# Kernel tuning notes

Hardware: AMD Instinct MI355X
Metric: run time of the kernel (lower is better)

## Reference

```python
import jax, jax.numpy as jnp
import numpy as np

B, N, H, BD, P = 16, 128, 128, 64, 256

def setup_inputs() -> dict:
    key = jax.random.key(0)
    ks = jax.random.split(key, 10)
    s = lambda fan_in: 1.0 / np.sqrt(fan_in)
    return {
        "hidden_states": jax.random.normal(ks[0], (B, N, H), dtype=jnp.float32),
        "positions": jax.random.normal(ks[1], (B, N, 2), dtype=jnp.float32),
        "W1": jax.random.uniform(ks[2], (2, BD), jnp.float32, -s(2), s(2)),
        "b1": jax.random.uniform(ks[3], (BD,), jnp.float32, -s(2), s(2)),
        "W2": jax.random.uniform(ks[4], (H + BD, P), jnp.float32, -s(H + BD), s(H + BD)),
        "b2": jax.random.uniform(ks[5], (P,), jnp.float32, -s(H + BD), s(H + BD)),
        "W3": jax.random.uniform(ks[6], (P, P), jnp.float32, -s(P), s(P)),
        "b3": jax.random.uniform(ks[7], (P,), jnp.float32, -s(P), s(P)),
        "Wout": jax.random.uniform(ks[8], (P, P), jnp.float32, -s(P), s(P)),
        "bout": jax.random.uniform(ks[9], (P,), jnp.float32, -s(P), s(P)),
    }

def reference(hidden_states, positions, W1, b1, W2, b2, W3, b3, Wout, bout):
    b, n, h = hidden_states.shape
    # rel[b,i,j] = pos[b,j] - pos[b,i]  -> [B,N,N,2]
    rel = positions[:, None, :, :] - positions[:, :, None, :]
    enc = jax.nn.relu(rel @ W1 + b1)                       # [B,N,N,BD]
    hid = jnp.broadcast_to(hidden_states[:, None, :, :], (b, n, n, h))
    x = jnp.concatenate([hid, enc], axis=-1)               # [B,N,N,H+BD]
    emb = jax.nn.relu(x @ W2 + b2) @ W3 + b3               # [B,N,N,P]
    # mask self (j == i) with -inf before max-pool over neighbors j
    self_mask = jnp.eye(n, dtype=bool)[None, :, :, None]
    emb = jnp.where(self_mask, -jnp.inf, emb)
    pooled = emb.max(axis=2)                               # [B,N,P]
    return pooled @ Wout + bout
```

## Files before the change

### kernel.cpp

```cpp
#include <hip/hip_runtime.h>
#include <hip/hip_fp16.h>

using f16x4 = __attribute__((ext_vector_type(4))) _Float16;
using f16x8 = __attribute__((ext_vector_type(8))) _Float16;
using f32x4 = __attribute__((ext_vector_type(4))) float;

__device__ __forceinline__ f16x4 ld_f16x4(const void* p) {
    return *reinterpret_cast<const f16x4*>(p);
}
__device__ __forceinline__ f16x8 ld_f16x8(const void* p) {
    return *reinterpret_cast<const f16x8*>(p);
}

__global__ void sp_wconv(const float* __restrict__ W2, const float* __restrict__ W3,
                         const float* __restrict__ pos, const float* __restrict__ W1,
                         const float* __restrict__ b1,
                         _Float16* __restrict__ W2bt, _Float16* __restrict__ W3s,
                         _Float16* __restrict__ T1h, _Float16* __restrict__ T1bh) {
    int t = blockIdx.x * 256 + threadIdx.x;
    if (t < 16384) {
        int p = t >> 6, k = t & 63;
        W2bt[t] = (_Float16)W2[(128 + k) * 256 + p];
    }
    {
        int ks = t >> 13, rem = t & 8191;
        int row = rem >> 5, inner = rem & 31;
        int slot = inner >> 3, e = inner & 7;
        int g = slot ^ ((row >> 1) & 3);
        int k = ks * 32 + ((e & 4) << 2) + (g << 2) + (e & 3);
        W3s[t] = (_Float16)W3[k * 256 + row];
    }
#pragma unroll
    for (int h = 0; h < 2; ++h) {
        int idx = t + h * 65536;
        int row = idx >> 6, k = idx & 63;
        float v = pos[row * 2] * W1[k] + pos[row * 2 + 1] * W1[64 + k];
        T1h[idx]  = (_Float16)v;
        T1bh[idx] = (_Float16)(v + b1[k]);
    }
}

__global__ void sp_hpart(const float* __restrict__ hs, const float* __restrict__ W2,
                         const float* __restrict__ b2, _Float16* __restrict__ hp16) {
    __shared__ float sh[8 * 128];
    int rb = blockIdx.x * 8;
    int tid = threadIdx.x;
    for (int t = tid; t < 1024; t += 256) sh[t] = hs[rb * 128 + t];
    __syncthreads();
    float acc[8];
    float bb = b2[tid];
#pragma unroll
    for (int r = 0; r < 8; ++r) acc[r] = bb;
    for (int k = 0; k < 128; ++k) {
        float w = W2[k * 256 + tid];
#pragma unroll
        for (int r = 0; r < 8; ++r) acc[r] += sh[r * 128 + k] * w;
    }
#pragma unroll
    for (int r = 0; r < 8; ++r) hp16[(rb + r) * 256 + tid] = (_Float16)acc[r];
}

__global__ __launch_bounds__(256, 2) void sp_main(
    const float* __restrict__ b3,
    const _Float16* __restrict__ hp16, const _Float16* __restrict__ W2bt,
    const _Float16* __restrict__ W3s, const _Float16* __restrict__ T1h,
    const _Float16* __restrict__ T1bh, float* __restrict__ pool) {
    __shared__ __align__(16) char sW3[8][8192];
    __shared__ _Float16 sPoolH[4][8][128];

    const int bid = blockIdx.x;
    const int ig = bid & 15, ph = (bid >> 4) & 1, b = bid >> 5;
    const int tid = threadIdx.x;
    const int wj = tid >> 6, lane = tid & 63;
    const int l15 = lane & 15, lk = lane >> 4;

    {
        const uint4* W3v = (const uint4*)W3s + ph * 512;
        uint4* dst = (uint4*)sW3;
#pragma unroll
        for (int c = 0; c < 16; ++c) {
            dst[c * 256 + tid] = W3v[c * 256 + tid + (c >> 1) * 512];
        }
    }

    f16x8 tb[2][2];
#pragma unroll
    for (int jt = 0; jt < 2; ++jt) {
        int j = wj * 32 + jt * 16 + l15;
        const _Float16* tj = T1bh + (b * 128 + j) * 64 + lk * 8;
        tb[jt][0] = ld_f16x8(tj);
        tb[jt][1] = ld_f16x8(tj + 32);
    }

    const _Float16* hpb = hp16 + (b * 128 + wj * 32 + l15) * 256 + lk * 4;
    const _Float16* tib = T1h + (b * 128) * 64 + lk * 8;
    const int slot = lk ^ ((l15 >> 1) & 3);

    __syncthreads();

#pragma unroll 1
    for (int ii2 = 0; ii2 < 4; ++ii2) {
        const int i0 = ig * 8 + ii2 * 2;
        const int i1 = i0 + 1;

        const _Float16* w2p = W2bt;
        const _Float16* hpp = hpb;
        asm volatile("" : "+v"(w2p), "+v"(hpp));

        f16x8 benc[2][2][2];
#pragma unroll
        for (int iq = 0; iq < 2; ++iq) {
            const int i = iq ? i1 : i0;
#pragma unroll
            for (int s32 = 0; s32 < 2; ++s32) {
                f16x8 cv = ld_f16x8(tib + i * 64 + s32 * 32);
#pragma unroll
                for (int jt = 0; jt < 2; ++jt) {
                    f16x8 v;
#pragma unroll
                    for (int e = 0; e < 8; ++e) {
                        _Float16 d = tb[jt][s32][e] - cv[e];
                        v[e] = d > (_Float16)0 ? d : (_Float16)0;
                    }
                    benc[iq][jt][s32] = v;
                }
            }
        }

        f32x4 eacc[2][2][8];
#pragma unroll
        for (int iq = 0; iq < 2; ++iq)
#pragma unroll
            for (int jt = 0; jt < 2; ++jt)
#pragma unroll
                for (int pt = 0; pt < 8; ++pt)
                    eacc[iq][jt][pt] = (f32x4){0.f, 0.f, 0.f, 0.f};

#pragma unroll
        for (int ks = 0; ks < 8; ++ks) {
            f16x8 u[2][2];
#pragma unroll
            for (int pp = 0; pp < 2; ++pp) {
                const int pt = ks * 2 + pp;
                f32x4 a[2][2];
#pragma unroll
                for (int iq = 0; iq < 2; ++iq)
#pragma unroll
                    for (int jt = 0; jt < 2; ++jt) a[iq][jt] = (f32x4){0.f, 0.f, 0.f, 0.f};
#pragma unroll
                for (int s32 = 0; s32 < 2; ++s32) {
                    f16x8 aw = ld_f16x8(w2p + (pt * 16 + l15) * 64 + s32 * 32 + lk * 8);
                    a[0][0] = __builtin_amdgcn_mfma_f32_16x16x32_f16(aw, benc[0][0][s32], a[0][0], 0, 0, 0);
                    a[0][1] = __builtin_amdgcn_mfma_f32_16x16x32_f16(aw, benc[0][1][s32], a[0][1], 0, 0, 0);
                    a[1][0] = __builtin_amdgcn_mfma_f32_16x16x32_f16(aw, benc[1][0][s32], a[1][0], 0, 0, 0);
                    a[1][1] = __builtin_amdgcn_mfma_f32_16x16x32_f16(aw, benc[1][1][s32], a[1][1], 0, 0, 0);
                }
                f16x4 h0 = ld_f16x4(hpp + pt * 16);
                f16x4 h1 = ld_f16x4(hpp + 16 * 256 + pt * 16);
#pragma unroll
                for (int iq = 0; iq < 2; ++iq)
#pragma unroll
                    for (int r = 0; r < 4; ++r) {
                        float t0 = a[iq][0][r] + (float)h0[r];
                        float t1 = a[iq][1][r] + (float)h1[r];
                        u[iq][0][pp * 4 + r] = (_Float16)(t0 > 0.f ? t0 : 0.f);
                        u[iq][1][pp * 4 + r] = (_Float16)(t1 > 0.f ? t1 : 0.f);
                    }
            }
#pragma unroll
            for (int pt = 0; pt < 8; ++pt) {
                f16x8 bf = ld_f16x8(sW3[ks] + (pt * 16 + l15) * 64 + slot * 16);
                eacc[0][0][pt] = __builtin_amdgcn_mfma_f32_16x16x32_f16(u[0][0], bf, eacc[0][0][pt], 0, 0, 0);
                eacc[0][1][pt] = __builtin_amdgcn_mfma_f32_16x16x32_f16(u[0][1], bf, eacc[0][1][pt], 0, 0, 0);
                eacc[1][0][pt] = __builtin_amdgcn_mfma_f32_16x16x32_f16(u[1][0], bf, eacc[1][0][pt], 0, 0, 0);
                eacc[1][1][pt] = __builtin_amdgcn_mfma_f32_16x16x32_f16(u[1][1], bf, eacc[1][1][pt], 0, 0, 0);
            }
        }

#pragma unroll
        for (int iq = 0; iq < 2; ++iq) {
            const int i = iq ? i1 : i0;
#pragma unroll
            for (int pt = 0; pt < 8; ++pt) {
                float m = -INFINITY;
#pragma unroll
                for (int jt = 0; jt < 2; ++jt) {
#pragma unroll
                    for (int r = 0; r < 4; ++r) {
                        int row = wj * 32 + jt * 16 + lk * 4 + r;
                        float v = eacc[iq][jt][pt][r];
                        if (row != i) m = fmaxf(m, v);
                    }
                }
                m = fmaxf(m, __shfl_xor(m, 16));
                m = fmaxf(m, __shfl_xor(m, 32));
                if (lane < 16) sPoolH[wj][ii2 * 2 + iq][pt * 16 + l15] = (_Float16)m;
            }
        }
    }
    __syncthreads();

#pragma unroll
    for (int q = 0; q < 4; ++q) {
        int idx = q * 256 + tid;
        int ii = idx >> 7, t = idx & 127;
        float v = fmaxf(fmaxf((float)sPoolH[0][ii][t], (float)sPoolH[1][ii][t]),
                        fmaxf((float)sPoolH[2][ii][t], (float)sPoolH[3][ii][t]));
        int p = ph * 128 + t;
        pool[(b * 128 + ig * 8 + ii) * 256 + p] = v + b3[p];
    }
}

__global__ void sp_out(const float* __restrict__ Wout, const float* __restrict__ bout,
                       float* __restrict__ io) {
    __shared__ float sp[8 * 256];
    int rb = blockIdx.x * 8;
    int tid = threadIdx.x;
    for (int t = tid; t < 2048; t += 256) sp[t] = io[rb * 256 + t];
    __syncthreads();
    float acc[8];
    float bb = bout[tid];
#pragma unroll
    for (int r = 0; r < 8; ++r) acc[r] = bb;
    for (int k = 0; k < 256; ++k) {
        float w = Wout[k * 256 + tid];
#pragma unroll
        for (int r = 0; r < 8; ++r) acc[r] += sp[r * 256 + k] * w;
    }
#pragma unroll
    for (int r = 0; r < 8; ++r) io[(rb + r) * 256 + tid] = acc[r];
}

extern "C" void kernel_launch(void* const* d_in, const int* in_sizes, int n_in,
                              void* d_out, int out_size, void* d_ws, size_t ws_size,
                              hipStream_t stream) {
    const float* hs   = (const float*)d_in[0];
    const float* pos  = (const float*)d_in[1];
    const float* W1   = (const float*)d_in[2];
    const float* b1   = (const float*)d_in[3];
    const float* W2   = (const float*)d_in[4];
    const float* b2   = (const float*)d_in[5];
    const float* W3   = (const float*)d_in[6];
    const float* b3   = (const float*)d_in[7];
    const float* Wout = (const float*)d_in[8];
    const float* bout = (const float*)d_in[9];
    float* out = (float*)d_out;

    _Float16* hp16 = (_Float16*)d_ws;
    _Float16* W2bt = (_Float16*)((char*)d_ws + (1 << 20));
    _Float16* W3s  = (_Float16*)((char*)d_ws + (1 << 20) + 32768);
    _Float16* T1h  = (_Float16*)((char*)d_ws + (1 << 20) + 32768 + 131072);
    _Float16* T1bh = (_Float16*)((char*)d_ws + (1 << 20) + 32768 + 131072 + 262144);

    sp_wconv<<<256, 256, 0, stream>>>(W2, W3, pos, W1, b1, W2bt, W3s, T1h, T1bh);
    sp_hpart<<<256, 256, 0, stream>>>(hs, W2, b2, hp16);
    sp_main<<<512, 256, 0, stream>>>(b3, hp16, W2bt, W3s, T1h, T1bh, out);
    sp_out<<<256, 256, 0, stream>>>(Wout, bout, out);
}
```

Before: 99.73 us.

## Switch main kernel MFMAs from 16x16x32 to 32x32x16 tiles

Rewrites the fused two-layer MLP inner loop to use 32x32x16 f16 MFMA instructions instead of 16x16x32, with a matching re-swizzle of the W3 shared-memory layout and of the lane-to-row mappings for the encoding, hidden-part and pooling steps. The larger tiles are meant to reduce operand loads and instruction count per FLOP and to cut the cross-lane shuffles in the max-pool. The bias-add and ReLU on the first-layer output are now done in half precision rather than float, which loses some accuracy. The larger accumulator tiles also raise register pressure under the 2-blocks-per-CU launch bound.

```diff
diff --git a/kernel.cpp b/kernel.cpp
--- a/kernel.cpp
+++ b/kernel.cpp
@@ -4,6 +4,7 @@
 using f16x4 = __attribute__((ext_vector_type(4))) _Float16;
 using f16x8 = __attribute__((ext_vector_type(8))) _Float16;
 using f32x4 = __attribute__((ext_vector_type(4))) float;
+using f32x16 = __attribute__((ext_vector_type(16))) float;
 
 __device__ __forceinline__ f16x4 ld_f16x4(const void* p) {
     return *reinterpret_cast<const f16x4*>(p);
@@ -23,11 +24,11 @@
         W2bt[t] = (_Float16)W2[(128 + k) * 256 + p];
     }
     {
-        int ks = t >> 13, rem = t & 8191;
-        int row = rem >> 5, inner = rem & 31;
+        int kk = t >> 12, rem = t & 4095;
+        int row = rem >> 4, inner = rem & 15;
         int slot = inner >> 3, e = inner & 7;
-        int g = slot ^ ((row >> 1) & 3);
-        int k = ks * 32 + ((e & 4) << 2) + (g << 2) + (e & 3);
+        int h = slot ^ ((row >> 2) & 1);
+        int k = kk * 16 + (e & 3) + 8 * (e >> 2) + 4 * h;
         W3s[t] = (_Float16)W3[k * 256 + row];
     }
 #pragma unroll
@@ -65,36 +66,28 @@
     const _Float16* __restrict__ hp16, const _Float16* __restrict__ W2bt,
     const _Float16* __restrict__ W3s, const _Float16* __restrict__ T1h,
     const _Float16* __restrict__ T1bh, float* __restrict__ pool) {
-    __shared__ __align__(16) char sW3[8][8192];
+    __shared__ __align__(16) char sW3[16][4096];
     __shared__ _Float16 sPoolH[4][8][128];
 
     const int bid = blockIdx.x;
     const int ig = bid & 15, ph = (bid >> 4) & 1, b = bid >> 5;
     const int tid = threadIdx.x;
     const int wj = tid >> 6, lane = tid & 63;
-    const int l15 = lane & 15, lk = lane >> 4;
+    const int l31 = lane & 31, hi = lane >> 5;
 
     {
-        const uint4* W3v = (const uint4*)W3s + ph * 512;
+        const uint4* W3v = (const uint4*)W3s;
         uint4* dst = (uint4*)sW3;
 #pragma unroll
-        for (int c = 0; c < 16; ++c) {
-            dst[c * 256 + tid] = W3v[c * 256 + tid + (c >> 1) * 512];
-        }
-    }
-
-    f16x8 tb[2][2];
-#pragma unroll
-    for (int jt = 0; jt < 2; ++jt) {
-        int j = wj * 32 + jt * 16 + l15;
-        const _Float16* tj = T1bh + (b * 128 + j) * 64 + lk * 8;
-        tb[jt][0] = ld_f16x8(tj);
-        tb[jt][1] = ld_f16x8(tj + 32);
-    }
-
-    const _Float16* hpb = hp16 + (b * 128 + wj * 32 + l15) * 256 + lk * 4;
-    const _Float16* tib = T1h + (b * 128) * 64 + lk * 8;
-    const int slot = lk ^ ((l15 >> 1) & 3);
+        for (int c = 0; c < 16; ++c)
+            dst[c * 256 + tid] = W3v[c * 512 + ph * 256 + tid];
+    }
+
+    const int jl = wj * 32 + l31;
+    const _Float16* tjb = T1bh + (b * 128 + jl) * 64 + hi * 8;
+    const _Float16* tib = T1h + (b * 128) * 64 + hi * 8;
+    const _Float16* hpb = hp16 + (b * 128 + jl) * 256;
+    const int slotB = (hi ^ ((l31 >> 2) & 1)) * 16;
 
     __syncthreads();
 
@@ -107,94 +100,83 @@
         const _Float16* hpp = hpb;
         asm volatile("" : "+v"(w2p), "+v"(hpp));
 
-        f16x8 benc[2][2][2];
+        f16x8 benc[2][4];
+#pragma unroll
+        for (int s = 0; s < 4; ++s) {
+            f16x8 tbv = ld_f16x8(tjb + s * 16);
+            f16x8 cv0 = ld_f16x8(tib + i0 * 64 + s * 16);
+            f16x8 cv1 = ld_f16x8(tib + i1 * 64 + s * 16);
+#pragma unroll
+            for (int e = 0; e < 8; ++e) {
+                _Float16 d0 = tbv[e] - cv0[e];
+                _Float16 d1 = tbv[e] - cv1[e];
+                benc[0][s][e] = d0 > (_Float16)0 ? d0 : (_Float16)0;
+                benc[1][s][e] = d1 > (_Float16)0 ? d1 : (_Float16)0;
+            }
+        }
+
+        f32x16 eacc[2][4];
+#pragma unroll
+        for (int iq = 0; iq < 2; ++iq)
+#pragma unroll
+            for (int nt = 0; nt < 4; ++nt)
+#pragma unroll
+                for (int r = 0; r < 16; ++r) eacc[iq][nt][r] = 0.f;
+
+#pragma unroll
+        for (int t = 0; t < 8; ++t) {
+            f32x16 a0, a1;
+#pragma unroll
+            for (int r = 0; r < 16; ++r) { a0[r] = 0.f; a1[r] = 0.f; }
+#pragma unroll
+            for (int s = 0; s < 4; ++s) {
+                f16x8 aw = ld_f16x8(w2p + (t * 32 + l31) * 64 + s * 16 + hi * 8);
+                a0 = __builtin_amdgcn_mfma_f32_32x32x16_f16(aw, benc[0][s], a0, 0, 0, 0);
+                a1 = __builtin_amdgcn_mfma_f32_32x32x16_f16(aw, benc[1][s], a1, 0, 0, 0);
+            }
+            f16x4 hp0 = ld_f16x4(hpp + t * 32 + 4 * hi);
+            f16x4 hp1 = ld_f16x4(hpp + t * 32 + 8 + 4 * hi);
+            f16x4 hp2 = ld_f16x4(hpp + t * 32 + 16 + 4 * hi);
+            f16x4 hp3 = ld_f16x4(hpp + t * 32 + 24 + 4 * hi);
+            f16x8 u00, u01, u10, u11;
+#pragma unroll
+            for (int e = 0; e < 4; ++e) {
+                _Float16 v;
+                v = (_Float16)a0[e]      + hp0[e]; u00[e]     = v > (_Float16)0 ? v : (_Float16)0;
+                v = (_Float16)a0[e + 4]  + hp1[e]; u00[e + 4] = v > (_Float16)0 ? v : (_Float16)0;
+                v = (_Float16)a0[e + 8]  + hp2[e]; u01[e]     = v > (_Float16)0 ? v : (_Float16)0;
+                v = (_Float16)a0[e + 12] + hp3[e]; u01[e + 4] = v > (_Float16)0 ? v : (_Float16)0;
+                v = (_Float16)a1[e]      + hp0[e]; u10[e]     = v > (_Float16)0 ? v : (_Float16)0;
+                v = (_Float16)a1[e + 4]  + hp1[e]; u10[e + 4] = v > (_Float16)0 ? v : (_Float16)0;
+                v = (_Float16)a1[e + 8]  + hp2[e]; u11[e]     = v > (_Float16)0 ? v : (_Float16)0;
+                v = (_Float16)a1[e + 12] + hp3[e]; u11[e + 4] = v > (_Float16)0 ? v : (_Float16)0;
+            }
+#pragma unroll
+            for (int nt = 0; nt < 4; ++nt) {
+                const char* rowp = (const char*)sW3 + (nt * 32 + l31) * 32 + slotB;
+                f16x8 bf0 = ld_f16x8(rowp + (2 * t) * 4096);
+                f16x8 bf1 = ld_f16x8(rowp + (2 * t + 1) * 4096);
+                eacc[0][nt] = __builtin_amdgcn_mfma_f32_32x32x16_f16(u00, bf0, eacc[0][nt], 0, 0, 0);
+                eacc[1][nt] = __builtin_amdgcn_mfma_f32_32x32x16_f16(u10, bf0, eacc[1][nt], 0, 0, 0);
+                eacc[0][nt] = __builtin_amdgcn_mfma_f32_32x32x16_f16(u01, bf1, eacc[0][nt], 0, 0, 0);
+                eacc[1][nt] = __builtin_amdgcn_mfma_f32_32x32x16_f16(u11, bf1, eacc[1][nt], 0, 0, 0);
+            }
+        }
+
 #pragma unroll
         for (int iq = 0; iq < 2; ++iq) {
             const int i = iq ? i1 : i0;
 #pragma unroll
-            for (int s32 = 0; s32 < 2; ++s32) {
-                f16x8 cv = ld_f16x8(tib + i * 64 + s32 * 32);
-#pragma unroll
-                for (int jt = 0; jt < 2; ++jt) {
-                    f16x8 v;
-#pragma unroll
-                    for (int e = 0; e < 8; ++e) {
-                        _Float16 d = tb[jt][s32][e] - cv[e];
-                        v[e] = d > (_Float16)0 ? d : (_Float16)0;
-                    }
-                    benc[iq][jt][s32] = v;
+            for (int nt = 0; nt < 4; ++nt) {
+                float m = -INFINITY;
+#pragma unroll
+                for (int r = 0; r < 16; ++r) {
+                    int jrow = wj * 32 + (r & 3) + 8 * (r >> 2) + 4 * hi;
+                    float v = eacc[iq][nt][r];
+                    if (jrow != i) m = fmaxf(m, v);
                 }
-            }
-        }
-
-        f32x4 eacc[2][2][8];
-#pragma unroll
-        for (int iq = 0; iq < 2; ++iq)
-#pragma unroll
-            for (int jt = 0; jt < 2; ++jt)
-#pragma unroll
-                for (int pt = 0; pt < 8; ++pt)
-                    eacc[iq][jt][pt] = (f32x4){0.f, 0.f, 0.f, 0.f};
-
-#pragma unroll
-        for (int ks = 0; ks < 8; ++ks) {
-            f16x8 u[2][2];
-#pragma unroll
-            for (int pp = 0; pp < 2; ++pp) {
-                const int pt = ks * 2 + pp;
-                f32x4 a[2][2];
-#pragma unroll
-                for (int iq = 0; iq < 2; ++iq)
-#pragma unroll
-                    for (int jt = 0; jt < 2; ++jt) a[iq][jt] = (f32x4){0.f, 0.f, 0.f, 0.f};
-#pragma unroll
-                for (int s32 = 0; s32 < 2; ++s32) {
-                    f16x8 aw = ld_f16x8(w2p + (pt * 16 + l15) * 64 + s32 * 32 + lk * 8);
-                    a[0][0] = __builtin_amdgcn_mfma_f32_16x16x32_f16(aw, benc[0][0][s32], a[0][0], 0, 0, 0);
-                    a[0][1] = __builtin_amdgcn_mfma_f32_16x16x32_f16(aw, benc[0][1][s32], a[0][1], 0, 0, 0);
-                    a[1][0] = __builtin_amdgcn_mfma_f32_16x16x32_f16(aw, benc[1][0][s32], a[1][0], 0, 0, 0);
-                    a[1][1] = __builtin_amdgcn_mfma_f32_16x16x32_f16(aw, benc[1][1][s32], a[1][1], 0, 0, 0);
-                }
-                f16x4 h0 = ld_f16x4(hpp + pt * 16);
-                f16x4 h1 = ld_f16x4(hpp + 16 * 256 + pt * 16);
-#pragma unroll
-                for (int iq = 0; iq < 2; ++iq)
-#pragma unroll
-                    for (int r = 0; r < 4; ++r) {
-                        float t0 = a[iq][0][r] + (float)h0[r];
-                        float t1 = a[iq][1][r] + (float)h1[r];
-                        u[iq][0][pp * 4 + r] = (_Float16)(t0 > 0.f ? t0 : 0.f);
-                        u[iq][1][pp * 4 + r] = (_Float16)(t1 > 0.f ? t1 : 0.f);
-                    }
-            }
-#pragma unroll
-            for (int pt = 0; pt < 8; ++pt) {
-                f16x8 bf = ld_f16x8(sW3[ks] + (pt * 16 + l15) * 64 + slot * 16);
-                eacc[0][0][pt] = __builtin_amdgcn_mfma_f32_16x16x32_f16(u[0][0], bf, eacc[0][0][pt], 0, 0, 0);
-                eacc[0][1][pt] = __builtin_amdgcn_mfma_f32_16x16x32_f16(u[0][1], bf, eacc[0][1][pt], 0, 0, 0);
-                eacc[1][0][pt] = __builtin_amdgcn_mfma_f32_16x16x32_f16(u[1][0], bf, eacc[1][0][pt], 0, 0, 0);
-                eacc[1][1][pt] = __builtin_amdgcn_mfma_f32_16x16x32_f16(u[1][1], bf, eacc[1][1][pt], 0, 0, 0);
-            }
-        }
-
-#pragma unroll
-        for (int iq = 0; iq < 2; ++iq) {
-            const int i = iq ? i1 : i0;
-#pragma unroll
-            for (int pt = 0; pt < 8; ++pt) {
-                float m = -INFINITY;
-#pragma unroll
-                for (int jt = 0; jt < 2; ++jt) {
-#pragma unroll
-                    for (int r = 0; r < 4; ++r) {
-                        int row = wj * 32 + jt * 16 + lk * 4 + r;
-                        float v = eacc[iq][jt][pt][r];
-                        if (row != i) m = fmaxf(m, v);
-                    }
-                }
-                m = fmaxf(m, __shfl_xor(m, 16));
                 m = fmaxf(m, __shfl_xor(m, 32));
-                if (lane < 16) sPoolH[wj][ii2 * 2 + iq][pt * 16 + l15] = (_Float16)m;
+                if (lane < 32) sPoolH[wj][ii2 * 2 + iq][nt * 32 + l31] = (_Float16)m;
             }
         }
     }
```

After: 94.91 us. 4.8% less time.
